# Kernel optimization log

Hardware: AMD Instinct MI355X
Metric: run time of the kernel (lower is better)

Reference implementation:

```python
import jax, jax.numpy as jnp
import numpy as np

DIM = 192
HEADS = 8
B, H, W = 8, 128, 128


def _split_heads(t, heads):
    # [b, n, c] -> [b, heads, c//heads, n]
    b, n, c = t.shape
    t = t.reshape(b, n, heads, c // heads)
    return jnp.transpose(t, (0, 2, 3, 1))


def _l2norm(t):
    # normalize along last (token) dim, matching F.normalize eps=1e-12
    n = jnp.linalg.norm(t, axis=-1, keepdims=True)
    return t / jnp.maximum(n, 1e-12)


def setup_inputs() -> dict:
    key = jax.random.key(0)
    ks = jax.random.split(key, 12)
    s = 1.0 / np.sqrt(DIM)
    inp = {
        "x1": jax.random.normal(ks[0], (B, DIM, H, W), jnp.float32),
        "x2": jax.random.normal(ks[1], (B, DIM, H, W), jnp.float32),
        "q1": jax.random.normal(ks[2], (B, DIM, H, W), jnp.float32),
        "q2": jax.random.normal(ks[3], (B, DIM, H, W), jnp.float32),
        "Wq": jax.random.normal(ks[4], (DIM, DIM), jnp.float32) * s,
        "bq": jax.random.normal(ks[5], (DIM,), jnp.float32) * s,
        "Wk": jax.random.normal(ks[6], (DIM, DIM), jnp.float32) * s,
        "bk": jax.random.normal(ks[7], (DIM,), jnp.float32) * s,
        "Wv": jax.random.normal(ks[8], (DIM, DIM), jnp.float32) * s,
        "bv": jax.random.normal(ks[9], (DIM,), jnp.float32) * s,
        "scale": jnp.ones((HEADS, 1, 1), jnp.float32),
        "Wproj": jax.random.normal(ks[10], (DIM, DIM), jnp.float32) * s,
    }
    return inp


def reference(x1, x2, q1, q2, Wq, bq, Wk, bk, Wv, bv, scale, Wproj):
    b, c, h, w = x1.shape
    heads = HEADS

    def flat(t):  # b c h w -> b (h w) c
        return jnp.transpose(t.reshape(b, c, h * w), (0, 2, 1))

    x1f, x2f, q1f, q2f = flat(x1), flat(x2), flat(q1), flat(q2)

    # NOTE: faithful to source: q2 uses q_proj1; k2/v2 use k_proj1/v_proj1
    q1p = q1f @ Wq.T + bq
    q2p = q2f @ Wq.T + bq
    k1 = x1f @ Wk.T + bk
    v1 = x1f @ Wv.T + bv
    k2 = x2f @ Wk.T + bk
    v2 = x2f @ Wv.T + bv

    q1h = _l2norm(_split_heads(q1p, heads))  # [b, head, hd, n]
    q2h = _l2norm(_split_heads(q2p, heads))
    k1h = _l2norm(_split_heads(k1, heads))
    k2h = _l2norm(_split_heads(k2, heads))
    v1h = _split_heads(v1, heads)
    v2h = _split_heads(v2, heads)

    # channel attention: [b, head, hd, hd]
    attn1 = jax.nn.softmax(jnp.einsum('bhcn,bhdn->bhcd', q1h, k2h) * scale, axis=-1)
    out1 = jnp.einsum('bhcd,bhdn->bhcn', attn1, v2h)
    attn2 = jax.nn.softmax(jnp.einsum('bhcn,bhdn->bhcd', q2h, k1h) * scale, axis=-1)
    out2 = jnp.einsum('bhcd,bhdn->bhcn', attn2, v1h)

    def merge(t):  # [b, head, hd, n] -> [b, c, h, w]
        return t.reshape(b, c, h, w)

    out1 = jnp.einsum('oc,bchw->bohw', Wproj, merge(out1))
    out2 = jnp.einsum('oc,bchw->bohw', Wproj, merge(out2))
    return (out1, out2)
```

## Files before the change

kernel.cpp:

```cpp
#include <hip/hip_runtime.h>
#include <hip/hip_bf16.h>
#include <math.h>

using bf16 = __hip_bfloat16;
typedef __attribute__((ext_vector_type(8))) short short8;
typedef __attribute__((ext_vector_type(4))) short short4v;
typedef __attribute__((ext_vector_type(4))) float f32x4;

static __device__ __forceinline__ bf16 f2b(float x) { return __float2bfloat16(x); }
static __device__ __forceinline__ short f2bs(float x) {
  bf16 h = __float2bfloat16(x);
  return *reinterpret_cast<short*>(&h);
}

#define MFMA16(a, b, c) __builtin_amdgcn_mfma_f32_16x16x32_bf16((a), (b), (c), 0, 0, 0)

#define NB 8
#define CDIM 192
#define NTOK 16384
#define CN ((size_t)CDIM * NTOK)

__global__ __launch_bounds__(256) void convert_w(const float* __restrict__ Wq,
                                                 const float* __restrict__ Wk,
                                                 bf16* __restrict__ Wqk) {
  const int e = (blockIdx.x * 256 + threadIdx.x) * 4;
  const float* src = (e < CDIM * CDIM) ? (Wq + e) : (Wk + (e - CDIM * CDIM));
  f32x4 v = *reinterpret_cast<const f32x4*>(src);
  short4v w;
  w[0] = f2bs(v[0]); w[1] = f2bs(v[1]); w[2] = f2bs(v[2]); w[3] = f2bs(v[3]);
  *reinterpret_cast<short4v*>(Wqk + e) = w;
}

struct GemmParams {
  const float *q1, *q2, *x1, *x2;
  const bf16* Wqk;
  const float *bq, *bk;
  bf16* proj;
  const bf16* M;
  const float* Bf;
  float* out;
  int mode;
};

__global__ __launch_bounds__(256, 4) void gemm_oc(GemmParams P) {
  const int tid = threadIdx.x;
  const int z = blockIdx.y;

  const float* Xf;
  const bf16* Wb;
  const float* bias;
  bf16* OUTb = nullptr;
  float* OUTf = nullptr;

  if (P.mode == 0) {
    const int b = z >> 2, p = z & 3;
    Xf = (p == 0 ? P.q1 : p == 1 ? P.q2 : p == 2 ? P.x1 : P.x2) + (size_t)b * CN;
    Wb = P.Wqk + ((p < 2) ? 0 : CDIM * CDIM);
    bias = (p < 2) ? P.bq : P.bk;
    OUTb = P.proj + (size_t)(p * 8 + b) * CN;
  } else {
    Wb = P.M + (size_t)z * (CDIM * CDIM);
    bias = P.Bf + z * CDIM;
    Xf = (((z >> 3) == 0) ? P.x2 : P.x1) + (size_t)(z & 7) * CN;
    OUTf = P.out + (size_t)z * CN;
  }

  const int n0 = blockIdx.x * 64;

  __shared__ __align__(16) bf16 Xs[64 * 200];

  {
    const int c0 = (tid & 15) * 4;
    const int t0 = (tid >> 4) * 4;
    f32x4 v[3][4];
#pragma unroll
    for (int cb = 0; cb < 3; cb++)
#pragma unroll
      for (int i = 0; i < 4; i++)
        v[cb][i] = *reinterpret_cast<const f32x4*>(
            Xf + (size_t)(cb * 64 + c0 + i) * NTOK + n0 + t0);
#pragma unroll
    for (int cb = 0; cb < 3; cb++) {
#pragma unroll
      for (int j = 0; j < 4; j++) {
        short4v w;
        w[0] = f2bs(v[cb][0][j]);
        w[1] = f2bs(v[cb][1][j]);
        w[2] = f2bs(v[cb][2][j]);
        w[3] = f2bs(v[cb][3][j]);
        *reinterpret_cast<short4v*>(&Xs[(t0 + j) * 200 + cb * 64 + c0]) = w;
      }
    }
  }
  __syncthreads();

  const int lane = tid & 63, wave = tid >> 6;
  const int quad = lane >> 4, l15 = lane & 15;
  const int ob = wave * 48;

  f32x4 acc[4][3];
#pragma unroll
  for (int t = 0; t < 4; t++)
#pragma unroll
    for (int ot = 0; ot < 3; ot++) acc[t][ot] = (f32x4){0.f, 0.f, 0.f, 0.f};

  const bf16* W0 = Wb + (size_t)(ob + l15) * CDIM;

#pragma unroll
  for (int ks = 0; ks < 6; ks++) {
    const int k0 = ks * 32 + quad * 8;
    short8 xf[4], wf[3];
#pragma unroll
    for (int t = 0; t < 4; t++)
      xf[t] = *reinterpret_cast<const short8*>(&Xs[(t * 16 + l15) * 200 + k0]);
#pragma unroll
    for (int ot = 0; ot < 3; ot++)
      wf[ot] = *reinterpret_cast<const short8*>(W0 + (size_t)ot * 16 * CDIM + k0);
#pragma unroll
    for (int t = 0; t < 4; t++)
#pragma unroll
      for (int ot = 0; ot < 3; ot++) acc[t][ot] = MFMA16(xf[t], wf[ot], acc[t][ot]);
  }

#pragma unroll
  for (int ot = 0; ot < 3; ot++) {
    const int o = ob + ot * 16 + l15;
    const float bo = bias[o];
    if (P.mode == 0) {
      bf16* dst = OUTb + (size_t)o * NTOK + n0 + quad * 4;
#pragma unroll
      for (int t = 0; t < 4; t++) {
        short4v w;
        w[0] = f2bs(acc[t][ot][0] + bo);
        w[1] = f2bs(acc[t][ot][1] + bo);
        w[2] = f2bs(acc[t][ot][2] + bo);
        w[3] = f2bs(acc[t][ot][3] + bo);
        *reinterpret_cast<short4v*>(dst + t * 16) = w;
      }
    } else {
      float* dst = OUTf + (size_t)o * NTOK + n0 + quad * 4;
#pragma unroll
      for (int t = 0; t < 4; t++) {
        f32x4 w = {acc[t][ot][0] + bo, acc[t][ot][1] + bo,
                   acc[t][ot][2] + bo, acc[t][ot][3] + bo};
        *reinterpret_cast<f32x4*>(dst + t * 16) = w;
      }
    }
  }
}

__global__ __launch_bounds__(256, 2) void gram48(const bf16* __restrict__ proj,
                                                 float* __restrict__ Gbuf) {
  const int blk = blockIdx.x;
  const int ks = blk & 3, h = (blk >> 2) & 7, b = (blk >> 5) & 7, p = blk >> 8;

  const bf16* qsel = proj + (size_t)((p == 0 ? 0 : 1) * 8 + b) * CN + (size_t)h * 24 * NTOK;
  const bf16* ksel = proj + (size_t)((p == 0 ? 3 : 2) * 8 + b) * CN + (size_t)h * 24 * NTOK;

  const int tid = threadIdx.x, wave = tid >> 6, lane = tid & 63;
  const int quad = lane >> 4, l15 = lane & 15;

  const bf16* rp[3];
#pragma unroll
  for (int mt = 0; mt < 3; mt++) {
    int r = mt * 16 + l15;
    rp[mt] = (r < 24) ? qsel + (size_t)r * NTOK : ksel + (size_t)(r - 24) * NTOK;
  }

  f32x4 acc[3][3];
#pragma unroll
  for (int i = 0; i < 3; i++)
#pragma unroll
    for (int j = 0; j < 3; j++) acc[i][j] = (f32x4){0.f, 0.f, 0.f, 0.f};

  const int kend = ks * 4096 + 4096;
#pragma unroll 2
  for (int k = ks * 4096 + wave * 32 + quad * 8; k < kend; k += 128) {
    short8 f[3];
#pragma unroll
    for (int mt = 0; mt < 3; mt++) f[mt] = *reinterpret_cast<const short8*>(rp[mt] + k);
#pragma unroll
    for (int i = 0; i < 3; i++)
#pragma unroll
      for (int j = 0; j < 3; j++) acc[i][j] = MFMA16(f[i], f[j], acc[i][j]);
  }

  __shared__ float Gs[48 * 48];
  for (int i = tid; i < 2304; i += 256) Gs[i] = 0.f;
  __syncthreads();
#pragma unroll
  for (int i = 0; i < 3; i++)
#pragma unroll
    for (int j = 0; j < 3; j++)
#pragma unroll
      for (int r = 0; r < 4; r++)
        atomicAdd(&Gs[(i * 16 + quad * 4 + r) * 48 + j * 16 + l15], acc[i][j][r]);
  __syncthreads();

  float* gout = Gbuf + (size_t)((p * 8 + b) * 8 + h) * 2304;
  for (int i = tid; i < 2304; i += 256) atomicAdd(gout + i, Gs[i]);
}

__global__ void attn_softmax(const float* __restrict__ Gbuf, const float* __restrict__ scale,
                             float* __restrict__ Abuf) {
  const int blk = blockIdx.x;
  const int h = blk & 7;
  const float* G = Gbuf + (size_t)blk * 2304;
  __shared__ float nrm[48];
  const int t = threadIdx.x;
  if (t < 48) nrm[t] = sqrtf(fmaxf(G[t * 48 + t], 0.f));
  __syncthreads();
  if (t < 24) {
    const float scl = scale[h];
    const float nq = fmaxf(nrm[t], 1e-12f);
    float lg[24], mx = -1e30f;
#pragma unroll
    for (int d = 0; d < 24; d++) {
      lg[d] = G[t * 48 + 24 + d] / (nq * fmaxf(nrm[24 + d], 1e-12f)) * scl;
      mx = fmaxf(mx, lg[d]);
    }
    float s = 0.f;
#pragma unroll
    for (int d = 0; d < 24; d++) { lg[d] = expf(lg[d] - mx); s += lg[d]; }
    const float inv = 1.f / s;
    float* Ao = Abuf + (size_t)blk * 576 + t * 24;
#pragma unroll
    for (int d = 0; d < 24; d++) Ao[d] = lg[d] * inv;
  }
}

__global__ __launch_bounds__(256) void fold_M(const float* __restrict__ Abuf,
                                              const float* __restrict__ Wproj,
                                              const float* __restrict__ Wv,
                                              const float* __restrict__ bv,
                                              bf16* __restrict__ Mbuf,
                                              float* __restrict__ Bbuf) {
  const int blk = blockIdx.x;
  const int pb = blk / 12, ot = blk % 12;
  const int tid = threadIdx.x;

  __shared__ float As[4608];
  __shared__ float Wps[3072];
  __shared__ float Ts[3072];
  __shared__ float bvs[192];

  for (int i = tid; i < 4608; i += 256) As[i] = Abuf[(size_t)pb * 4608 + i];
  for (int i = tid; i < 3072; i += 256)
    Wps[i] = Wproj[(size_t)(ot * 16 + i / 192) * CDIM + (i % 192)];
  if (tid < 192) bvs[tid] = bv[tid];
  __syncthreads();

  for (int idx = tid; idx < 3072; idx += 256) {
    const int tr = idx / 192, cp = idx % 192;
    const int h = cp / 24, d = cp % 24;
    const float* Ah = &As[h * 576 + d];
    const float* Wr = &Wps[tr * 192 + h * 24];
    float s = 0.f;
#pragma unroll
    for (int cl = 0; cl < 24; cl++) s += Wr[cl] * Ah[cl * 24];
    Ts[idx] = s;
  }
  __syncthreads();

  for (int idx = tid; idx < 3072; idx += 256) {
    const int tr = idx / 192, e = idx % 192;
    const float* Tr = &Ts[tr * 192];
    float s = 0.f;
#pragma unroll 8
    for (int cp = 0; cp < 192; cp++) s += Tr[cp] * Wv[(size_t)cp * CDIM + e];
    Mbuf[((size_t)pb * CDIM + ot * 16 + tr) * CDIM + e] = f2b(s);
  }
  if (tid < 16) {
    const float* Tr = &Ts[tid * 192];
    float s = 0.f;
#pragma unroll 8
    for (int cp = 0; cp < 192; cp++) s += Tr[cp] * bvs[cp];
    Bbuf[pb * CDIM + ot * 16 + tid] = s;
  }
}

extern "C" void kernel_launch(void* const* d_in, const int* in_sizes, int n_in,
                              void* d_out, int out_size, void* d_ws, size_t ws_size,
                              hipStream_t stream) {
  const float* x1 = (const float*)d_in[0];
  const float* x2 = (const float*)d_in[1];
  const float* q1 = (const float*)d_in[2];
  const float* q2 = (const float*)d_in[3];
  const float* Wq = (const float*)d_in[4];
  const float* bq = (const float*)d_in[5];
  const float* Wk = (const float*)d_in[6];
  const float* bk = (const float*)d_in[7];
  const float* Wv = (const float*)d_in[8];
  const float* bv = (const float*)d_in[9];
  const float* scale = (const float*)d_in[10];
  const float* Wproj = (const float*)d_in[11];

  char* ws = (char*)d_ws;
  const size_t proj_bytes = (size_t)4 * 8 * CN * 2;
  const size_t gbuf_bytes = (size_t)2 * 8 * 8 * 2304 * 4;
  const size_t abuf_bytes = (size_t)2 * 8 * 8 * 576 * 4;
  const size_t mbuf_bytes = (size_t)16 * 192 * 192 * 2;

  bf16* proj = (bf16*)ws;
  float* Gbuf = (float*)(ws + proj_bytes);
  float* Abuf = (float*)(ws + proj_bytes + gbuf_bytes);
  bf16* Mbuf = (bf16*)(ws + proj_bytes + gbuf_bytes + abuf_bytes);
  float* Bbuf = (float*)(ws + proj_bytes + gbuf_bytes + abuf_bytes + mbuf_bytes);
  bf16* Wqk = (bf16*)(ws + proj_bytes + gbuf_bytes);
  Wqk = (bf16*)Abuf;

  hipMemsetAsync(Gbuf, 0, gbuf_bytes, stream);

  convert_w<<<dim3(72), 256, 0, stream>>>(Wq, Wk, Wqk);

  GemmParams P;
  P.q1 = q1; P.q2 = q2; P.x1 = x1; P.x2 = x2;
  P.Wqk = Wqk; P.bq = bq; P.bk = bk;
  P.proj = proj; P.M = Mbuf; P.Bf = Bbuf; P.out = (float*)d_out;
  P.mode = 0;

  gemm_oc<<<dim3(256, 32), 256, 0, stream>>>(P);
  gram48<<<dim3(512), 256, 0, stream>>>(proj, Gbuf);
  attn_softmax<<<dim3(128), 64, 0, stream>>>(Gbuf, scale, Abuf);
  fold_M<<<dim3(192), 256, 0, stream>>>(Abuf, Wproj, Wv, bv, Mbuf, Bbuf);
  GemmParams P2 = P; P2.mode = 1;
  gemm_oc<<<dim3(256, 16), 256, 0, stream>>>(P2);
}
```

Baseline: 771.9 us.

## Make projection GEMM persistent with double-buffered LDS prefetch; split Gram reduction finer

```diff
diff --git a/kernel.cpp b/kernel.cpp
--- a/kernel.cpp
+++ b/kernel.cpp
@@ -42,117 +42,144 @@
   int mode;
 };
 
-__global__ __launch_bounds__(256, 4) void gemm_oc(GemmParams P) {
+__global__ __launch_bounds__(256, 3) void gemm_oc(GemmParams P) {
   const int tid = threadIdx.x;
-  const int z = blockIdx.y;
-
-  const float* Xf;
-  const bf16* Wb;
-  const float* bias;
-  bf16* OUTb = nullptr;
-  float* OUTf = nullptr;
-
-  if (P.mode == 0) {
-    const int b = z >> 2, p = z & 3;
-    Xf = (p == 0 ? P.q1 : p == 1 ? P.q2 : p == 2 ? P.x1 : P.x2) + (size_t)b * CN;
-    Wb = P.Wqk + ((p < 2) ? 0 : CDIM * CDIM);
-    bias = (p < 2) ? P.bq : P.bk;
-    OUTb = P.proj + (size_t)(p * 8 + b) * CN;
-  } else {
-    Wb = P.M + (size_t)z * (CDIM * CDIM);
-    bias = P.Bf + z * CDIM;
-    Xf = (((z >> 3) == 0) ? P.x2 : P.x1) + (size_t)(z & 7) * CN;
-    OUTf = P.out + (size_t)z * CN;
-  }
-
-  const int n0 = blockIdx.x * 64;
-
-  __shared__ __align__(16) bf16 Xs[64 * 200];
-
-  {
-    const int c0 = (tid & 15) * 4;
-    const int t0 = (tid >> 4) * 4;
-    f32x4 v[3][4];
-#pragma unroll
-    for (int cb = 0; cb < 3; cb++)
-#pragma unroll
-      for (int i = 0; i < 4; i++)
-        v[cb][i] = *reinterpret_cast<const f32x4*>(
-            Xf + (size_t)(cb * 64 + c0 + i) * NTOK + n0 + t0);
-#pragma unroll
-    for (int cb = 0; cb < 3; cb++) {
-#pragma unroll
-      for (int j = 0; j < 4; j++) {
-        short4v w;
-        w[0] = f2bs(v[cb][0][j]);
-        w[1] = f2bs(v[cb][1][j]);
-        w[2] = f2bs(v[cb][2][j]);
-        w[3] = f2bs(v[cb][3][j]);
-        *reinterpret_cast<short4v*>(&Xs[(t0 + j) * 200 + cb * 64 + c0]) = w;
-      }
-    }
-  }
-  __syncthreads();
-
+  const int totalU = (P.mode == 0) ? 8192 : 4096;
+
+  const int c0 = (tid & 15) * 4;
+  const int t0 = (tid >> 4) * 4;
   const int lane = tid & 63, wave = tid >> 6;
   const int quad = lane >> 4, l15 = lane & 15;
   const int ob = wave * 48;
 
-  f32x4 acc[4][3];
-#pragma unroll
-  for (int t = 0; t < 4; t++)
-#pragma unroll
-    for (int ot = 0; ot < 3; ot++) acc[t][ot] = (f32x4){0.f, 0.f, 0.f, 0.f};
-
-  const bf16* W0 = Wb + (size_t)(ob + l15) * CDIM;
-
-#pragma unroll
-  for (int ks = 0; ks < 6; ks++) {
-    const int k0 = ks * 32 + quad * 8;
-    short8 xf[4], wf[3];
+  __shared__ __align__(16) bf16 Xs[2][64 * 200];
+
+  f32x4 v[12];
+
+  auto xptr = [&](int z) -> const float* {
+    if (P.mode == 0) {
+      const int b = z >> 2, p = z & 3;
+      return (p == 0 ? P.q1 : p == 1 ? P.q2 : p == 2 ? P.x1 : P.x2) + (size_t)b * CN;
+    }
+    return (((z >> 3) == 0) ? P.x2 : P.x1) + (size_t)(z & 7) * CN;
+  };
+  auto loadRegs = [&](int uu) {
+    const float* Xf = xptr(uu >> 8);
+    const int n0 = (uu & 255) * 64;
+#pragma unroll
+    for (int cb = 0; cb < 3; cb++)
+#pragma unroll
+      for (int i = 0; i < 4; i++)
+        v[cb * 4 + i] = *reinterpret_cast<const f32x4*>(
+            Xf + (size_t)(cb * 64 + c0 + i) * NTOK + n0 + t0);
+  };
+  auto writeLds = [&](int buf) {
+#pragma unroll
+    for (int cb = 0; cb < 3; cb++)
+#pragma unroll
+      for (int j = 0; j < 4; j++) {
+        short4v w;
+        w[0] = f2bs(v[cb * 4 + 0][j]);
+        w[1] = f2bs(v[cb * 4 + 1][j]);
+        w[2] = f2bs(v[cb * 4 + 2][j]);
+        w[3] = f2bs(v[cb * 4 + 3][j]);
+        *reinterpret_cast<short4v*>(&Xs[buf][(t0 + j) * 200 + cb * 64 + c0]) = w;
+      }
+  };
+
+  int u = blockIdx.x;
+  if (u >= totalU) return;
+
+  loadRegs(u);
+  writeLds(0);
+  __syncthreads();
+
+  int cur = 0;
+  while (true) {
+    const int z = u >> 8, n0 = (u & 255) * 64;
+    const int un = u + (int)gridDim.x;
+    const bool hasNext = (un < totalU);
+
+    if (hasNext) loadRegs(un);
+
+    const bf16* Wb;
+    const float* bias;
+    bf16* OUTb = nullptr;
+    float* OUTf = nullptr;
+    if (P.mode == 0) {
+      const int b = z >> 2, p = z & 3;
+      Wb = P.Wqk + ((p < 2) ? 0 : CDIM * CDIM);
+      bias = (p < 2) ? P.bq : P.bk;
+      OUTb = P.proj + (size_t)(p * 8 + b) * CN;
+    } else {
+      Wb = P.M + (size_t)z * (CDIM * CDIM);
+      bias = P.Bf + z * CDIM;
+      OUTf = P.out + (size_t)z * CN;
+    }
+
+    f32x4 acc[4][3];
 #pragma unroll
     for (int t = 0; t < 4; t++)
-      xf[t] = *reinterpret_cast<const short8*>(&Xs[(t * 16 + l15) * 200 + k0]);
-#pragma unroll
-    for (int ot = 0; ot < 3; ot++)
-      wf[ot] = *reinterpret_cast<const short8*>(W0 + (size_t)ot * 16 * CDIM + k0);
-#pragma unroll
-    for (int t = 0; t < 4; t++)
-#pragma unroll
-      for (int ot = 0; ot < 3; ot++) acc[t][ot] = MFMA16(xf[t], wf[ot], acc[t][ot]);
-  }
-
-#pragma unroll
-  for (int ot = 0; ot < 3; ot++) {
-    const int o = ob + ot * 16 + l15;
-    const float bo = bias[o];
-    if (P.mode == 0) {
-      bf16* dst = OUTb + (size_t)o * NTOK + n0 + quad * 4;
-#pragma unroll
-      for (int t = 0; t < 4; t++) {
-        short4v w;
-        w[0] = f2bs(acc[t][ot][0] + bo);
-        w[1] = f2bs(acc[t][ot][1] + bo);
-        w[2] = f2bs(acc[t][ot][2] + bo);
-        w[3] = f2bs(acc[t][ot][3] + bo);
-        *reinterpret_cast<short4v*>(dst + t * 16) = w;
+#pragma unroll
+      for (int ot = 0; ot < 3; ot++) acc[t][ot] = (f32x4){0.f, 0.f, 0.f, 0.f};
+
+    const bf16* W0 = Wb + (size_t)(ob + l15) * CDIM;
+
+#pragma unroll
+    for (int ks = 0; ks < 6; ks++) {
+      const int k0 = ks * 32 + quad * 8;
+      short8 xf[4], wf[3];
+#pragma unroll
+      for (int t = 0; t < 4; t++)
+        xf[t] = *reinterpret_cast<const short8*>(&Xs[cur][(t * 16 + l15) * 200 + k0]);
+#pragma unroll
+      for (int ot = 0; ot < 3; ot++)
+        wf[ot] = *reinterpret_cast<const short8*>(W0 + (size_t)ot * 16 * CDIM + k0);
+#pragma unroll
+      for (int t = 0; t < 4; t++)
+#pragma unroll
+        for (int ot = 0; ot < 3; ot++) acc[t][ot] = MFMA16(xf[t], wf[ot], acc[t][ot]);
+    }
+
+    if (hasNext) writeLds(cur ^ 1);
+
+#pragma unroll
+    for (int ot = 0; ot < 3; ot++) {
+      const int o = ob + ot * 16 + l15;
+      const float bo = bias[o];
+      if (P.mode == 0) {
+        bf16* dst = OUTb + (size_t)o * NTOK + n0 + quad * 4;
+#pragma unroll
+        for (int t = 0; t < 4; t++) {
+          short4v w;
+          w[0] = f2bs(acc[t][ot][0] + bo);
+          w[1] = f2bs(acc[t][ot][1] + bo);
+          w[2] = f2bs(acc[t][ot][2] + bo);
+          w[3] = f2bs(acc[t][ot][3] + bo);
+          *reinterpret_cast<short4v*>(dst + t * 16) = w;
+        }
+      } else {
+        float* dst = OUTf + (size_t)o * NTOK + n0 + quad * 4;
+#pragma unroll
+        for (int t = 0; t < 4; t++) {
+          f32x4 w = {acc[t][ot][0] + bo, acc[t][ot][1] + bo,
+                     acc[t][ot][2] + bo, acc[t][ot][3] + bo};
+          *reinterpret_cast<f32x4*>(dst + t * 16) = w;
+        }
       }
-    } else {
-      float* dst = OUTf + (size_t)o * NTOK + n0 + quad * 4;
-#pragma unroll
-      for (int t = 0; t < 4; t++) {
-        f32x4 w = {acc[t][ot][0] + bo, acc[t][ot][1] + bo,
-                   acc[t][ot][2] + bo, acc[t][ot][3] + bo};
-        *reinterpret_cast<f32x4*>(dst + t * 16) = w;
-      }
-    }
-  }
-}
-
-__global__ __launch_bounds__(256, 2) void gram48(const bf16* __restrict__ proj,
+    }
+
+    if (!hasNext) break;
+    __syncthreads();
+    cur ^= 1;
+    u = un;
+  }
+}
+
+__global__ __launch_bounds__(256, 4) void gram48(const bf16* __restrict__ proj,
                                                  float* __restrict__ Gbuf) {
   const int blk = blockIdx.x;
-  const int ks = blk & 3, h = (blk >> 2) & 7, b = (blk >> 5) & 7, p = blk >> 8;
+  const int ks = blk & 7, h = (blk >> 3) & 7, b = (blk >> 6) & 7, p = blk >> 9;
 
   const bf16* qsel = proj + (size_t)((p == 0 ? 0 : 1) * 8 + b) * CN + (size_t)h * 24 * NTOK;
   const bf16* ksel = proj + (size_t)((p == 0 ? 3 : 2) * 8 + b) * CN + (size_t)h * 24 * NTOK;
@@ -173,9 +200,9 @@
 #pragma unroll
     for (int j = 0; j < 3; j++) acc[i][j] = (f32x4){0.f, 0.f, 0.f, 0.f};
 
-  const int kend = ks * 4096 + 4096;
+  const int kend = ks * 2048 + 2048;
 #pragma unroll 2
-  for (int k = ks * 4096 + wave * 32 + quad * 8; k < kend; k += 128) {
+  for (int k = ks * 2048 + wave * 32 + quad * 8; k < kend; k += 128) {
     short8 f[3];
 #pragma unroll
     for (int mt = 0; mt < 3; mt++) f[mt] = *reinterpret_cast<const short8*>(rp[mt] + k);
@@ -306,8 +333,7 @@
   float* Abuf = (float*)(ws + proj_bytes + gbuf_bytes);
   bf16* Mbuf = (bf16*)(ws + proj_bytes + gbuf_bytes + abuf_bytes);
   float* Bbuf = (float*)(ws + proj_bytes + gbuf_bytes + abuf_bytes + mbuf_bytes);
-  bf16* Wqk = (bf16*)(ws + proj_bytes + gbuf_bytes);
-  Wqk = (bf16*)Abuf;
+  bf16* Wqk = (bf16*)Abuf;
 
   hipMemsetAsync(Gbuf, 0, gbuf_bytes, stream);
 
@@ -319,10 +345,10 @@
   P.proj = proj; P.M = Mbuf; P.Bf = Bbuf; P.out = (float*)d_out;
   P.mode = 0;
 
-  gemm_oc<<<dim3(256, 32), 256, 0, stream>>>(P);
-  gram48<<<dim3(512), 256, 0, stream>>>(proj, Gbuf);
+  gemm_oc<<<dim3(768), 256, 0, stream>>>(P);
+  gram48<<<dim3(1024), 256, 0, stream>>>(proj, Gbuf);
   attn_softmax<<<dim3(128), 64, 0, stream>>>(Gbuf, scale, Abuf);
   fold_M<<<dim3(192), 256, 0, stream>>>(Abuf, Wproj, Wv, bv, Mbuf, Bbuf);
   GemmParams P2 = P; P2.mode = 1;
-  gemm_oc<<<dim3(256, 16), 256, 0, stream>>>(P2);
-}
+  gemm_oc<<<dim3(768), 256, 0, stream>>>(P2);
+}
```

New measurement: 836.5 us. 8.4% more time.

## Permute channel layout for coalesced X loads and stage gram inputs through LDS

Applied to the files above, without the earlier changes.

```diff
diff --git a/kernel.cpp b/kernel.cpp
--- a/kernel.cpp
+++ b/kernel.cpp
@@ -20,15 +20,17 @@
 #define NTOK 16384
 #define CN ((size_t)CDIM * NTOK)
 
+#define CPERM(c) (((c) & 15) * 12 + ((c) >> 4))
+
 __global__ __launch_bounds__(256) void convert_w(const float* __restrict__ Wq,
                                                  const float* __restrict__ Wk,
                                                  bf16* __restrict__ Wqk) {
-  const int e = (blockIdx.x * 256 + threadIdx.x) * 4;
-  const float* src = (e < CDIM * CDIM) ? (Wq + e) : (Wk + (e - CDIM * CDIM));
-  f32x4 v = *reinterpret_cast<const f32x4*>(src);
-  short4v w;
-  w[0] = f2bs(v[0]); w[1] = f2bs(v[1]); w[2] = f2bs(v[2]); w[3] = f2bs(v[3]);
-  *reinterpret_cast<short4v*>(Wqk + e) = w;
+  const int g = blockIdx.x * 256 + threadIdx.x;
+  if (g >= 2 * CDIM * CDIM) return;
+  const int m = g / (CDIM * CDIM), rem = g % (CDIM * CDIM);
+  const int o = rem / CDIM, c = rem % CDIM;
+  const float v = (m == 0 ? Wq : Wk)[rem];
+  Wqk[m * CDIM * CDIM + o * CDIM + CPERM(c)] = f2b(v);
 }
 
 struct GemmParams {
@@ -70,25 +72,24 @@
   __shared__ __align__(16) bf16 Xs[64 * 200];
 
   {
-    const int c0 = (tid & 15) * 4;
-    const int t0 = (tid >> 4) * 4;
-    f32x4 v[3][4];
-#pragma unroll
-    for (int cb = 0; cb < 3; cb++)
-#pragma unroll
-      for (int i = 0; i < 4; i++)
-        v[cb][i] = *reinterpret_cast<const f32x4*>(
-            Xf + (size_t)(cb * 64 + c0 + i) * NTOK + n0 + t0);
-#pragma unroll
-    for (int cb = 0; cb < 3; cb++) {
-#pragma unroll
-      for (int j = 0; j < 4; j++) {
+    const int r = tid >> 4;
+    const int tc = (tid & 15) * 4;
+    f32x4 v[12];
+#pragma unroll
+    for (int ch = 0; ch < 12; ch++)
+      v[ch] = *reinterpret_cast<const f32x4*>(
+          Xf + (size_t)(ch * 16 + r) * NTOK + n0 + tc);
+#pragma unroll
+    for (int j = 0; j < 4; j++) {
+      const int rowb = (tc + j) * 200 + r * 12;
+#pragma unroll
+      for (int cb = 0; cb < 3; cb++) {
         short4v w;
-        w[0] = f2bs(v[cb][0][j]);
-        w[1] = f2bs(v[cb][1][j]);
-        w[2] = f2bs(v[cb][2][j]);
-        w[3] = f2bs(v[cb][3][j]);
-        *reinterpret_cast<short4v*>(&Xs[(t0 + j) * 200 + cb * 64 + c0]) = w;
+        w[0] = f2bs(v[cb * 4 + 0][j]);
+        w[1] = f2bs(v[cb * 4 + 1][j]);
+        w[2] = f2bs(v[cb * 4 + 2][j]);
+        w[3] = f2bs(v[cb * 4 + 3][j]);
+        *reinterpret_cast<short4v*>(&Xs[rowb + cb * 4]) = w;
       }
     }
   }
@@ -149,10 +150,12 @@
   }
 }
 
-__global__ __launch_bounds__(256, 2) void gram48(const bf16* __restrict__ proj,
+#define GS2 136
+
+__global__ __launch_bounds__(256, 4) void gram48(const bf16* __restrict__ proj,
                                                  float* __restrict__ Gbuf) {
   const int blk = blockIdx.x;
-  const int ks = blk & 3, h = (blk >> 2) & 7, b = (blk >> 5) & 7, p = blk >> 8;
+  const int ks = blk & 7, h = (blk >> 3) & 7, b = (blk >> 6) & 7, p = blk >> 9;
 
   const bf16* qsel = proj + (size_t)((p == 0 ? 0 : 1) * 8 + b) * CN + (size_t)h * 24 * NTOK;
   const bf16* ksel = proj + (size_t)((p == 0 ? 3 : 2) * 8 + b) * CN + (size_t)h * 24 * NTOK;
@@ -160,12 +163,19 @@
   const int tid = threadIdx.x, wave = tid >> 6, lane = tid & 63;
   const int quad = lane >> 4, l15 = lane & 15;
 
-  const bf16* rp[3];
-#pragma unroll
-  for (int mt = 0; mt < 3; mt++) {
-    int r = mt * 16 + l15;
-    rp[mt] = (r < 24) ? qsel + (size_t)r * NTOK : ksel + (size_t)(r - 24) * NTOK;
-  }
+  __shared__ __align__(16) bf16 Kt[2][48 * GS2];
+  __shared__ float Gs[48 * 48];
+
+  const int sr = tid >> 4, sc = (tid & 15) * 8;
+  const bf16* srcp[3];
+#pragma unroll
+  for (int ii = 0; ii < 3; ii++) {
+    const int r = ii * 16 + sr;
+    srcp[ii] = (r < 24 ? qsel + (size_t)r * NTOK : ksel + (size_t)(r - 24) * NTOK)
+               + ks * 2048 + sc;
+  }
+
+  for (int i = tid; i < 2304; i += 256) Gs[i] = 0.f;
 
   f32x4 acc[3][3];
 #pragma unroll
@@ -173,20 +183,39 @@
 #pragma unroll
     for (int j = 0; j < 3; j++) acc[i][j] = (f32x4){0.f, 0.f, 0.f, 0.f};
 
-  const int kend = ks * 4096 + 4096;
-#pragma unroll 2
-  for (int k = ks * 4096 + wave * 32 + quad * 8; k < kend; k += 128) {
+  short8 st[3];
+#pragma unroll
+  for (int ii = 0; ii < 3; ii++) st[ii] = *reinterpret_cast<const short8*>(srcp[ii]);
+#pragma unroll
+  for (int ii = 0; ii < 3; ii++)
+    *reinterpret_cast<short8*>(&Kt[0][(ii * 16 + sr) * GS2 + sc]) = st[ii];
+  __syncthreads();
+
+  const int kfrag = wave * 32 + quad * 8;
+  int cur = 0;
+  for (int t = 0; t < 16; t++) {
+    if (t < 15) {
+#pragma unroll
+      for (int ii = 0; ii < 3; ii++)
+        st[ii] = *reinterpret_cast<const short8*>(srcp[ii] + (t + 1) * 128);
+    }
     short8 f[3];
 #pragma unroll
-    for (int mt = 0; mt < 3; mt++) f[mt] = *reinterpret_cast<const short8*>(rp[mt] + k);
+    for (int mt = 0; mt < 3; mt++)
+      f[mt] = *reinterpret_cast<const short8*>(&Kt[cur][(mt * 16 + l15) * GS2 + kfrag]);
 #pragma unroll
     for (int i = 0; i < 3; i++)
 #pragma unroll
       for (int j = 0; j < 3; j++) acc[i][j] = MFMA16(f[i], f[j], acc[i][j]);
-  }
-
-  __shared__ float Gs[48 * 48];
-  for (int i = tid; i < 2304; i += 256) Gs[i] = 0.f;
+    if (t < 15) {
+#pragma unroll
+      for (int ii = 0; ii < 3; ii++)
+        *reinterpret_cast<short8*>(&Kt[cur ^ 1][(ii * 16 + sr) * GS2 + sc]) = st[ii];
+      __syncthreads();
+      cur ^= 1;
+    }
+  }
+
   __syncthreads();
 #pragma unroll
   for (int i = 0; i < 3; i++)
@@ -268,7 +297,7 @@
     float s = 0.f;
 #pragma unroll 8
     for (int cp = 0; cp < 192; cp++) s += Tr[cp] * Wv[(size_t)cp * CDIM + e];
-    Mbuf[((size_t)pb * CDIM + ot * 16 + tr) * CDIM + e] = f2b(s);
+    Mbuf[((size_t)pb * CDIM + ot * 16 + tr) * CDIM + CPERM(e)] = f2b(s);
   }
   if (tid < 16) {
     const float* Tr = &Ts[tid * 192];
@@ -306,12 +335,11 @@
   float* Abuf = (float*)(ws + proj_bytes + gbuf_bytes);
   bf16* Mbuf = (bf16*)(ws + proj_bytes + gbuf_bytes + abuf_bytes);
   float* Bbuf = (float*)(ws + proj_bytes + gbuf_bytes + abuf_bytes + mbuf_bytes);
-  bf16* Wqk = (bf16*)(ws + proj_bytes + gbuf_bytes);
-  Wqk = (bf16*)Abuf;
+  bf16* Wqk = (bf16*)Abuf;
 
   hipMemsetAsync(Gbuf, 0, gbuf_bytes, stream);
 
-  convert_w<<<dim3(72), 256, 0, stream>>>(Wq, Wk, Wqk);
+  convert_w<<<dim3(288), 256, 0, stream>>>(Wq, Wk, Wqk);
 
   GemmParams P;
   P.q1 = q1; P.q2 = q2; P.x1 = x1; P.x2 = x2;
@@ -320,7 +348,7 @@
   P.mode = 0;
 
   gemm_oc<<<dim3(256, 32), 256, 0, stream>>>(P);
-  gram48<<<dim3(512), 256, 0, stream>>>(proj, Gbuf);
+  gram48<<<dim3(1024), 256, 0, stream>>>(proj, Gbuf);
   attn_softmax<<<dim3(128), 64, 0, stream>>>(Gbuf, scale, Abuf);
   fold_M<<<dim3(192), 256, 0, stream>>>(Abuf, Wproj, Wv, bv, Mbuf, Bbuf);
   GemmParams P2 = P; P2.mode = 1;
```

Result: no change. 780.2 us (+1.1%).
